# Performance work log

Measured on AMD Instinct MI355X. Metric: run time of the kernel, lower is better.

Reference implementation:

```python
import jax, jax.numpy as jnp
import numpy as np

BN_EPS = 1e-5

def _conv(x, w, b, pad):
    # x [B,C,H,W], w [O,I,kh,kw]
    y = jax.lax.conv_general_dilated(x, w, window_strides=(1, 1),
                                     padding=[(pad, pad), (pad, pad)],
                                     dimension_numbers=('NCHW', 'OIHW', 'NCHW'))
    return y + b[None, :, None, None]

def _bn(x, p):
    # p [4,C] rows: gamma, beta, running_mean, running_var (inference-mode BN)
    g, b, m, v = p
    scale = (g * jax.lax.rsqrt(v + BN_EPS))[None, :, None, None]
    return (x - m[None, :, None, None]) * scale + b[None, :, None, None]

def _up2_bilinear_ac(x):
    # UpsamplingBilinear2d(scale_factor=2) == bilinear, align_corners=True
    def interp(x, axis):
        n = x.shape[axis]
        out = 2 * n
        c = jnp.arange(out, dtype=x.dtype) * ((n - 1) / (out - 1))
        i0 = jnp.floor(c).astype(jnp.int32)
        i1 = jnp.minimum(i0 + 1, n - 1)
        w = c - i0.astype(x.dtype)
        sh = [1] * x.ndim
        sh[axis] = out
        w = w.reshape(sh)
        return jnp.take(x, i0, axis=axis) * (1 - w) + jnp.take(x, i1, axis=axis) * w
    return interp(interp(x, 2), 3)

def _dilate(x, k, iterations):
    # cv2.dilate with ones(k,k) kernel == sliding-window max (the custom-kernel target);
    # get_open_map detaches, hence stop_gradient.
    for _ in range(iterations):
        x = jax.lax.reduce_window(x, -jnp.inf, jax.lax.max,
                                  (1, 1, k, k), (1, 1, 1, 1), 'SAME')
    return jax.lax.stop_gradient(x)

def _pixel_shuffle2(x):
    B, C4, H, W = x.shape
    C = C4 // 4
    x = x.reshape(B, C, 2, 2, H, W).transpose(0, 1, 4, 2, 5, 3)
    return x.reshape(B, C, 2 * H, 2 * W)

def setup_inputs() -> dict:
    key = jax.random.key(0)
    ks = jax.random.split(key, 16)
    B, C1, C2, H, W = 8, 64, 128, 64, 64

    def bn_params(k, C):
        k1, k2, k3, k4 = jax.random.split(k, 4)
        g = jax.random.uniform(k1, (C,)) * 0.5 + 0.75
        b = jax.random.normal(k2, (C,)) * 0.1
        m = jax.random.normal(k3, (C,)) * 0.1
        v = jax.random.uniform(k4, (C,)) + 0.5
        return jnp.stack([g, b, m, v])

    def conv_w(k, o, i, kk):
        return jax.random.normal(k, (o, i, kk, kk)) * 0.05

    return {
        'cur_x': jax.random.normal(ks[0], (B, C1, 2 * H, 2 * W)),
        'dep_x': jax.random.normal(ks[1], (B, C2, H, W)),
        'in_map': jax.random.normal(ks[2], (B, 1, H, W)),
        'up_w': conv_w(ks[3], 4 * C1, C2, 7), 'up_b': jnp.zeros((4 * C1,)),
        'up_bn': bn_params(ks[4], 4 * C1),
        'conv2_w': conv_w(ks[5], C1, C1, 3), 'conv2_b': jnp.zeros((C1,)),
        'd1_w': conv_w(ks[6], C1, C1, 3), 'd1_b': jnp.zeros((C1,)),
        'd1_bn': bn_params(ks[7], C1),
        'd2_w': conv_w(ks[8], C1, C1, 3), 'd2_b': jnp.zeros((C1,)),
        'd2_bn': bn_params(ks[9], C1),
        'd3_w': conv_w(ks[10], C1, C1, 3), 'd3_b': jnp.zeros((C1,)),
        'd3_bn': bn_params(ks[11], C1),
        'out_w': conv_w(ks[12], 1, C1, 7), 'out_b': jnp.zeros((1,)),
        'beta': jnp.ones((1,)),
    }

def reference(cur_x, dep_x, in_map, up_w, up_b, up_bn, conv2_w, conv2_b,
              d1_w, d1_b, d1_bn, d2_w, d2_b, d2_bn, d3_w, d3_b, d3_bn,
              out_w, out_b, beta):
    K, IT = 3, 1  # opr_kernel_size, iterations
    # up + pixel shuffle: [B,C2,H,W] -> [B,C1,2H,2W]
    dep = _pixel_shuffle2(jax.nn.relu(_bn(_conv(dep_x, up_w, up_b, 3), up_bn)))
    in_map1 = 1.0 - in_map
    input_map = jax.nn.sigmoid(_up2_bilinear_ac(in_map))
    input_map1 = jax.nn.sigmoid(_up2_bilinear_ac(in_map1))
    increase_map = _dilate(input_map, K, IT) - input_map
    increase_map1 = _dilate(increase_map, K, IT) - increase_map
    increase_map2 = _dilate(input_map1, K, IT) - input_map1
    outmap = increase_map + increase_map1 + increase_map2
    fn = _conv(outmap * cur_x, conv2_w, conv2_b, 1)
    r = jax.nn.relu(_bn(_conv(dep + beta * fn, d1_w, d1_b, 1), d1_bn))
    r = jax.nn.relu(_bn(_conv(r, d2_w, d2_b, 1), d2_bn))
    r = jax.nn.relu(_bn(_conv(r, d3_w, d3_b, 1), d3_bn))
    output_map = _conv(r, out_w, out_b, 3)
    return (r, output_map)
```

## Files before the change

### kernel.cpp

```cpp
#include <hip/hip_runtime.h>
#include <hip/hip_bf16.h>
#include <math.h>

static __device__ __forceinline__ float sigm(float x) { return 1.0f / (1.0f + expf(-x)); }

static __device__ __forceinline__ short f2bf_s(float f) {
    unsigned u = __float_as_uint(f);
    u += 0x7fffu + ((u >> 16) & 1u);
    return (short)(u >> 16);
}
static __device__ __forceinline__ float bfb2f(short s) {
    return __uint_as_float(((unsigned)(unsigned short)s) << 16);
}

typedef __attribute__((ext_vector_type(8))) short short8;
typedef __attribute__((ext_vector_type(4))) short short4v;
typedef __attribute__((ext_vector_type(4))) float f32x4;

static __device__ __forceinline__ void gl_lds16(const void* g, void* l) {
    __builtin_amdgcn_global_load_lds(
        (const __attribute__((address_space(1))) unsigned int*)g,
        (__attribute__((address_space(3))) unsigned int*)l, 16, 0, 0);
}

__global__ __launch_bounds__(256) void k_maps(const float* __restrict__ in_map,
                                              short* __restrict__ om_bf) {
    __shared__ float s_u[20][20];
    __shared__ float s_inc[18][18];
    int tid = threadIdx.x;
    int b = blockIdx.z;
    int ty0 = (blockIdx.x >> 3) << 4, tx0 = (blockIdx.x & 7) << 4;
    const float* p = in_map + (b << 12);
    const float s = 63.0f / 127.0f;
    for (int e = tid; e < 400; e += 256) {
        int yy = e / 20, xx = e % 20;
        int gy = ty0 + yy - 2, gx = tx0 + xx - 2;
        float v = 0.0f;
        if ((unsigned)gy < 128u && (unsigned)gx < 128u) {
            float cy = gy * s, cx = gx * s;
            int iy0 = (int)cy, ix0 = (int)cx;
            float wy = cy - (float)iy0, wx = cx - (float)ix0;
            int iy1 = min(iy0 + 1, 63), ix1 = min(ix0 + 1, 63);
            float v00 = p[(iy0 << 6) + ix0], v01 = p[(iy0 << 6) + ix1];
            float v10 = p[(iy1 << 6) + ix0], v11 = p[(iy1 << 6) + ix1];
            v = (1.0f - wy) * ((1.0f - wx) * v00 + wx * v01) +
                wy          * ((1.0f - wx) * v10 + wx * v11);
        }
        s_u[yy][xx] = v;
    }
    __syncthreads();
    for (int e = tid; e < 324; e += 256) {
        int yy = e / 18, xx = e % 18;
        int gy = ty0 + yy - 1, gx = tx0 + xx - 1;
        float val = -INFINITY;
        if ((unsigned)gy < 128u && (unsigned)gx < 128u) {
            float uc = s_u[yy + 1][xx + 1];
            float mx = -INFINITY;
            for (int dy = -1; dy <= 1; ++dy) {
                int ny = gy + dy; if ((unsigned)ny >= 128u) continue;
                for (int dx = -1; dx <= 1; ++dx) {
                    int nx = gx + dx; if ((unsigned)nx >= 128u) continue;
                    mx = fmaxf(mx, s_u[yy + 1 + dy][xx + 1 + dx]);
                }
            }
            val = sigm(mx) - sigm(uc);
        }
        s_inc[yy][xx] = val;
    }
    __syncthreads();
    int row = tid >> 4, col = tid & 15;
    int gy = ty0 + row, gx = tx0 + col;
    float mx = -INFINITY;
    #pragma unroll
    for (int dy = 0; dy < 3; ++dy)
        #pragma unroll
        for (int dx = 0; dx < 3; ++dx)
            mx = fmaxf(mx, s_inc[row + dy][col + dx]);
    float uc = s_u[row + 2][col + 2];
    float mn = INFINITY;
    for (int dy = -1; dy <= 1; ++dy) {
        int ny = gy + dy; if ((unsigned)ny >= 128u) continue;
        for (int dx = -1; dx <= 1; ++dx) {
            int nx = gx + dx; if ((unsigned)nx >= 128u) continue;
            mn = fminf(mn, s_u[row + 2 + dy][col + 2 + dx]);
        }
    }
    float inc2 = sigm(1.0f - mn) - sigm(1.0f - uc);
    om_bf[(b << 14) + (gy << 7) + gx] = f2bf_s(mx + inc2);
}

__global__ __launch_bounds__(256) void k_premult(const float* __restrict__ cur_x,
                                                 const short* __restrict__ om_bf,
                                                 short* __restrict__ xin2) {
    int e = blockIdx.x * 256 + threadIdx.x;
    int flat = e << 2;
    int pix = flat & 16383;
    int b = flat >> 20;
    f32x4 xv = *(const f32x4*)&cur_x[flat];
    short4v ov = *(const short4v*)&om_bf[(b << 14) + pix];
    short4v res;
    #pragma unroll
    for (int k = 0; k < 4; ++k) res[k] = f2bf_s(xv[k] * bfb2f(ov[k]));
    *(short4v*)&xin2[flat] = res;
}

__global__ __launch_bounds__(256) void k_prepw3(const float* __restrict__ w0,
                                                const float* __restrict__ w1,
                                                const float* __restrict__ w2,
                                                const float* __restrict__ w3,
                                                short* __restrict__ wb3) {
    int s = blockIdx.x * 256 + threadIdx.x;
    if (s >= 147456) return;
    int layer = s / 36864; int r = s - layer * 36864;
    const float* w = (layer == 0) ? w0 : (layer == 1) ? w1 : (layer == 2) ? w2 : w3;
    int o = r / 576; int rem = r - o * 576;
    int c = rem / 9; int t = rem - c * 9;
    int dy = t / 3, dx = t - dy * 3;
    int cc = c >> 5, cl = c & 31;
    wb3[layer * 36864 + (((cc * 3 + dx) * 3 + dy) * 64 + o) * 32 + cl] = f2bf_s(w[r]);
}

__global__ __launch_bounds__(256) void k_prepw(const float* __restrict__ w,
                                               short* __restrict__ wb) {
    int s = blockIdx.x * 256 + threadIdx.x;
    if (s >= 1605632) return;
    int O = s / 6272; int r = s - O * 6272;
    int C = r / 49;   int T = r - C * 49;
    int dy = T / 7, dx = T - dy * 7;
    int nt = O >> 6, o = O & 63;
    int cc = C >> 5, c = C & 31;
    int W = ((((nt * 4 + cc) * 7 + dx) * 7 + dy) * 64 + o) * 32 + c;
    wb[W] = f2bf_s(w[s]);
}

__global__ __launch_bounds__(256) void k_prepx(const float* __restrict__ x,
                                               short* __restrict__ px) {
    int b = blockIdx.z;
    int yp = blockIdx.x;
    int tid = threadIdx.x;
    int y = yp - 3;
    bool inY = (unsigned)y < 64u;
    for (int cc = 0; cc < 4; ++cc) {
        short* orow = px + (((long)(b * 4 + cc) * 70 + yp) * 70) * 40;
        for (int e = tid; e < 350; e += 256) {
            int p = e / 70, xp = e - p * 70;
            int xg = xp - 3;
            short8 v = (short8){0, 0, 0, 0, 0, 0, 0, 0};
            if (p < 4 && inY && (unsigned)xg < 64u) {
                const float* src = x + (((b * 128 + cc * 32 + p * 8) << 12)) + (y << 6) + xg;
                #pragma unroll
                for (int i = 0; i < 8; ++i) v[i] = f2bf_s(src[i << 12]);
            }
            *(short8*)&orow[xp * 40 + p * 8] = v;
        }
    }
}

__global__ __launch_bounds__(512, 4) void k_upconv_mfma(
    const short* __restrict__ px,
    const short* __restrict__ wb,
    const float* __restrict__ cb,
    const float* __restrict__ bnp,
    short* __restrict__ dep) {
    __shared__ __attribute__((aligned(16))) short s_in[19360];
    int tid = threadIdx.x;
    int wave = tid >> 6, lane = tid & 63;
    int q = lane >> 4, m = lane & 15;
    int mw = wave & 3, ng = wave >> 2;
    int ty0 = (blockIdx.x >> 2) * 16;
    int tx0 = (blockIdx.x & 3) * 16;
    int nt = blockIdx.y;
    int b = blockIdx.z;
    f32x4 acc[4][2];
    #pragma unroll
    for (int i = 0; i < 4; ++i)
        #pragma unroll
        for (int j = 0; j < 2; ++j)
            acc[i][j] = (f32x4){0.f, 0.f, 0.f, 0.f};

    auto stage = [&](int cc) {
        const short* pxcc = px + ((((long)(b * 4 + cc) * 70 + ty0) * 70 + tx0) * 40);
        for (int c0 = (wave << 6); c0 < 2420; c0 += 512) {
            int chunk = c0 + lane;
            int row = chunk / 110;
            int k = chunk - row * 110;
            if (chunk < 2420)
                gl_lds16(pxcc + row * 2800 + (k << 3), &s_in[c0 << 3]);
        }
    };

    for (int cc = 0; cc < 4; ++cc) {
        if (cc) __syncthreads();
        stage(cc);
        __syncthreads();
        const short* sb = &s_in[0];
        const short* wcc = wb + ((nt * 4 + cc) * 49) * 2048;
        #pragma unroll 1
        for (int dx = 0; dx < 7; ++dx) {
            short8 a10[10];
            #pragma unroll
            for (int r = 0; r < 10; ++r)
                a10[r] = *(const short8*)&sb[((mw * 4 + r) * 22 + m + dx) * 40 + q * 8];
            const short* wdx = wcc + ((dx * 7) << 11);
            short8 wf[7];
            #pragma unroll
            for (int dy = 0; dy < 7; ++dy)
                wf[dy] = *(const short8*)(wdx + (dy << 11) + ((ng * 32 + m) << 5) + (q << 3));
            #pragma unroll
            for (int dy = 0; dy < 7; ++dy)
                #pragma unroll
                for (int i = 0; i < 4; ++i)
                    acc[i][0] = __builtin_amdgcn_mfma_f32_16x16x32_bf16(
                        a10[i + dy], wf[dy], acc[i][0], 0, 0, 0);
            #pragma unroll
            for (int dy = 0; dy < 7; ++dy)
                wf[dy] = *(const short8*)(wdx + (dy << 11) + ((ng * 32 + 16 + m) << 5) + (q << 3));
            #pragma unroll
            for (int dy = 0; dy < 7; ++dy)
                #pragma unroll
                for (int i = 0; i < 4; ++i)
                    acc[i][1] = __builtin_amdgcn_mfma_f32_16x16x32_bf16(
                        a10[i + dy], wf[dy], acc[i][1], 0, 0, 0);
        }
    }
    #pragma unroll
    for (int j = 0; j < 2; ++j) {
        int o = nt * 64 + ng * 32 + j * 16 + m;
        float g  = bnp[o],       bt = bnp[256 + o];
        float mn = bnp[512 + o], vv = bnp[768 + o];
        float scale = g * rsqrtf(vv + 1e-5f);
        float cbf = cb[o];
        int c = o >> 2, sbit = (o >> 1) & 1, tbit = o & 1;
        #pragma unroll
        for (int i = 0; i < 4; ++i) {
            int y = ty0 + mw * 4 + i;
            #pragma unroll
            for (int reg = 0; reg < 4; ++reg) {
                int xc = tx0 + q * 4 + reg;
                float val = (acc[i][j][reg] + cbf - mn) * scale + bt;
                val = fmaxf(val, 0.0f);
                dep[((b * 64 + c) << 14) + ((2 * y + sbit) << 7) + (2 * xc + tbit)] = f2bf_s(val);
            }
        }
    }
}

template <int MODE, bool OUTBF>
__global__ __launch_bounds__(256, 4) void k_conv3m(
    const short* __restrict__ xin,
    const short* __restrict__ wl,
    const short* __restrict__ dep,
    const float* __restrict__ cb,
    const float* __restrict__ bnp,
    const float* __restrict__ beta,
    void* __restrict__ out) {
    __shared__ __attribute__((aligned(16))) short s_in[180 * 40];
    int tid = threadIdx.x;
    int wave = tid >> 6, lane = tid & 63;
    int q = lane >> 4, m = lane & 15;
    int mw = wave >> 1, nw = wave & 1;
    int ty0 = (blockIdx.x >> 3) * 8;
    int tx0 = (blockIdx.x & 7) * 16;
    int b = blockIdx.z;
    f32x4 acc[4][2];
    #pragma unroll
    for (int i = 0; i < 4; ++i)
        #pragma unroll
        for (int j = 0; j < 2; ++j)
            acc[i][j] = (f32x4){0.f, 0.f, 0.f, 0.f};
    const short* xb = xin + ((long)(b * 64) << 14);
    for (int cc = 0; cc < 2; ++cc) {
        __syncthreads();
        for (int e = tid; e < 240; e += 256) {
            int cq = e / 60; int rem = e - cq * 60;
            int yy = rem / 6; int g = rem - yy * 6;
            int gy = ty0 + yy - 1;
            int gx0 = tx0 - 4 + (g << 2);
            short4v v[8];
            if ((unsigned)gy < 128u && (unsigned)gx0 < 128u) {
                const short* src = xb + ((cc * 32 + cq * 8) << 14) + (gy << 7) + gx0;
                #pragma unroll
                for (int j2 = 0; j2 < 8; ++j2) v[j2] = *(const short4v*)(src + (j2 << 14));
            } else {
                #pragma unroll
                for (int j2 = 0; j2 < 8; ++j2) v[j2] = (short4v){0, 0, 0, 0};
            }
            #pragma unroll
            for (int t = 0; t < 4; ++t) {
                int xx = (g << 2) - 3 + t;
                if ((unsigned)xx < 18u) {
                    short8 pk;
                    #pragma unroll
                    for (int j2 = 0; j2 < 8; ++j2) pk[j2] = v[j2][t];
                    *(short8*)&s_in[(yy * 18 + xx) * 40 + cq * 8] = pk;
                }
            }
        }
        __syncthreads();
        #pragma unroll 1
        for (int dx = 0; dx < 3; ++dx) {
            short8 a6[6];
            #pragma unroll
            for (int r = 0; r < 6; ++r)
                a6[r] = *(const short8*)&s_in[((mw * 4 + r) * 18 + m + dx) * 40 + q * 8];
            const short* wdx = wl + (((cc * 3 + dx) * 3) << 11);
            short8 wf[3];
            #pragma unroll
            for (int dy = 0; dy < 3; ++dy)
                wf[dy] = *(const short8*)(wdx + (dy << 11) + ((nw * 32 + m) << 5) + (q << 3));
            #pragma unroll
            for (int dy = 0; dy < 3; ++dy)
                #pragma unroll
                for (int i = 0; i < 4; ++i)
                    acc[i][0] = __builtin_amdgcn_mfma_f32_16x16x32_bf16(
                        a6[i + dy], wf[dy], acc[i][0], 0, 0, 0);
            #pragma unroll
            for (int dy = 0; dy < 3; ++dy)
                wf[dy] = *(const short8*)(wdx + (dy << 11) + ((nw * 32 + 16 + m) << 5) + (q << 3));
            #pragma unroll
            for (int dy = 0; dy < 3; ++dy)
                #pragma unroll
                for (int i = 0; i < 4; ++i)
                    acc[i][1] = __builtin_amdgcn_mfma_f32_16x16x32_bf16(
                        a6[i + dy], wf[dy], acc[i][1], 0, 0, 0);
        }
    }
    float betav = (MODE == 1) ? beta[0] : 0.0f;
    #pragma unroll
    for (int j = 0; j < 2; ++j) {
        int o = nw * 32 + j * 16 + m;
        float cbf = cb[o];
        float scale = 1.0f, shift = 0.0f;
        if (MODE == 0) {
            float g  = bnp[o],       bt = bnp[64 + o];
            float mm = bnp[128 + o], vv = bnp[192 + o];
            scale = g * rsqrtf(vv + 1e-5f);
            shift = bt - mm * scale;
        }
        #pragma unroll
        for (int i = 0; i < 4; ++i) {
            int y = ty0 + mw * 4 + i;
            int base = ((b * 64 + o) << 14) + (y << 7) + tx0 + q * 4;
            float vals[4];
            if (MODE == 1) {
                short4v dv = *(const short4v*)&dep[base];
                #pragma unroll
                for (int reg = 0; reg < 4; ++reg)
                    vals[reg] = bfb2f(dv[reg]) + betav * (acc[i][j][reg] + cbf);
            } else {
                #pragma unroll
                for (int reg = 0; reg < 4; ++reg)
                    vals[reg] = fmaxf((acc[i][j][reg] + cbf) * scale + shift, 0.0f);
            }
            if (OUTBF) {
                short4v sv;
                #pragma unroll
                for (int reg = 0; reg < 4; ++reg) sv[reg] = f2bf_s(vals[reg]);
                *(short4v*)((short*)out + base) = sv;
            } else {
                f32x4 fv;
                #pragma unroll
                for (int reg = 0; reg < 4; ++reg) fv[reg] = vals[reg];
                *(f32x4*)((float*)out + base) = fv;
            }
        }
    }
}

__global__ __launch_bounds__(256) void k_outconv(
    const float* __restrict__ r,
    const float* __restrict__ w,
    const float* __restrict__ ob,
    float* __restrict__ out) {
    __shared__ float s_in[8][22][22];
    int tid = threadIdx.x;
    int ty = tid >> 4, tx = tid & 15;
    int ty0 = (blockIdx.x >> 3) << 4, tx0 = (blockIdx.x & 7) << 4;
    int b = blockIdx.z;
    float acc4[4] = {0.f, 0.f, 0.f, 0.f};
    for (int c0 = 0; c0 < 64; c0 += 8) {
        __syncthreads();
        for (int e = tid; e < 8 * 484; e += 256) {
            int i = e / 484; int r2 = e - i * 484; int yy = r2 / 22; int xx = r2 - yy * 22;
            int gy = ty0 + yy - 3, gx = tx0 + xx - 3;
            float v = 0.0f;
            if ((unsigned)gy < 128u && (unsigned)gx < 128u)
                v = r[((b * 64 + c0 + i) << 14) + (gy << 7) + gx];
            s_in[i][yy][xx] = v;
        }
        __syncthreads();
        for (int i = 0; i < 8; ++i) {
            const float* wrow = w + (c0 + i) * 49;
            #pragma unroll
            for (int dy = 0; dy < 7; ++dy)
                #pragma unroll
                for (int dx = 0; dx < 7; ++dx)
                    acc4[i & 3] = fmaf(s_in[i][ty + dy][tx + dx], wrow[dy * 7 + dx], acc4[i & 3]);
        }
    }
    out[(b << 14) + ((ty0 + ty) << 7) + tx0 + tx] =
        (acc4[0] + acc4[1]) + (acc4[2] + acc4[3]) + ob[0];
}

extern "C" void kernel_launch(void* const* d_in, const int* in_sizes, int n_in,
                              void* d_out, int out_size, void* d_ws, size_t ws_size,
                              hipStream_t stream) {
    const float* cur_x  = (const float*)d_in[0];
    const float* dep_x  = (const float*)d_in[1];
    const float* in_map = (const float*)d_in[2];
    const float* up_w   = (const float*)d_in[3];
    const float* up_b   = (const float*)d_in[4];
    const float* up_bn  = (const float*)d_in[5];
    const float* c2_w   = (const float*)d_in[6];
    const float* c2_b   = (const float*)d_in[7];
    const float* d1_w   = (const float*)d_in[8];
    const float* d1_b   = (const float*)d_in[9];
    const float* d1_bn  = (const float*)d_in[10];
    const float* d2_w   = (const float*)d_in[11];
    const float* d2_b   = (const float*)d_in[12];
    const float* d2_bn  = (const float*)d_in[13];
    const float* d3_w   = (const float*)d_in[14];
    const float* d3_b   = (const float*)d_in[15];
    const float* d3_bn  = (const float*)d_in[16];
    const float* out_w  = (const float*)d_in[17];
    const float* out_b  = (const float*)d_in[18];
    const float* beta   = (const float*)d_in[19];

    char* ob = (char*)d_out;
    float* r_out  = (float*)ob;
    short* A      = (short*)d_ws;
    short* B      = (short*)ob;
    short* C      = (short*)(ob + 16777216);
    short* wb     = C;
    short* px     = wb + 1605632;
    short* om_bf  = (short*)(ob + 33554432);
    short* wb3    = (short*)(ob + 33554432);
    float* mapout = (float*)(ob + 33554432);

    k_maps<<<dim3(64, 1, 8), 256, 0, stream>>>(in_map, om_bf);
    k_premult<<<8192, 256, 0, stream>>>(cur_x, om_bf, A);
    k_prepw3<<<576, 256, 0, stream>>>(c2_w, d1_w, d2_w, d3_w, wb3);
    k_prepw<<<6272, 256, 0, stream>>>(up_w, wb);
    k_prepx<<<dim3(70, 1, 8), 256, 0, stream>>>(dep_x, px);
    k_upconv_mfma<<<dim3(16, 4, 8), 512, 0, stream>>>(px, wb, up_b, up_bn, B);
    k_conv3m<1, true><<<dim3(128, 1, 8), 256, 0, stream>>>(
        A, wb3 + 0 * 36864, B, c2_b, nullptr, beta, C);
    k_conv3m<0, true><<<dim3(128, 1, 8), 256, 0, stream>>>(
        C, wb3 + 1 * 36864, nullptr, d1_b, d1_bn, nullptr, B);
    k_conv3m<0, true><<<dim3(128, 1, 8), 256, 0, stream>>>(
        B, wb3 + 2 * 36864, nullptr, d2_b, d2_bn, nullptr, A);
    k_conv3m<0, false><<<dim3(128, 1, 8), 256, 0, stream>>>(
        A, wb3 + 3 * 36864, nullptr, d3_b, d3_bn, nullptr, r_out);
    k_outconv<<<dim3(64, 1, 8), 256, 0, stream>>>(r_out, out_w, out_b, mapout);
}
```

Baseline: 465.0 us.

## Merge prep kernels into one launch and retile 3x3 convs to 16-row tiles

Folds the map, weight-reorder, and input-padding prep kernels into a single kernel that dispatches work by block index, removing three launches. The 3x3 conv kernel now uses 512 threads covering a 16x16 tile, loads all 64 input channels into LDS once with a single barrier, and splits output channels across wave groups. This cuts launch overhead and the per-channel-chunk sync and reload in the conv, at the cost of a much larger LDS footprint per block (about 57KB), which may lower occupancy. The om_bf buffer is moved to a new offset in the scratch space.

```diff
diff --git a/kernel.cpp b/kernel.cpp
--- a/kernel.cpp
+++ b/kernel.cpp
@@ -23,70 +23,117 @@
         (__attribute__((address_space(3))) unsigned int*)l, 16, 0, 0);
 }
 
-__global__ __launch_bounds__(256) void k_maps(const float* __restrict__ in_map,
-                                              short* __restrict__ om_bf) {
+__global__ __launch_bounds__(256) void k_prep_all(
+    const float* __restrict__ in_map, short* __restrict__ om_bf,
+    const float* __restrict__ w0, const float* __restrict__ w1,
+    const float* __restrict__ w2, const float* __restrict__ w3,
+    short* __restrict__ wb3,
+    const float* __restrict__ up_w, short* __restrict__ wb,
+    const float* __restrict__ dep_x, short* __restrict__ px) {
     __shared__ float s_u[20][20];
     __shared__ float s_inc[18][18];
+    int blk = blockIdx.x;
     int tid = threadIdx.x;
-    int b = blockIdx.z;
-    int ty0 = (blockIdx.x >> 3) << 4, tx0 = (blockIdx.x & 7) << 4;
-    const float* p = in_map + (b << 12);
-    const float s = 63.0f / 127.0f;
-    for (int e = tid; e < 400; e += 256) {
-        int yy = e / 20, xx = e % 20;
-        int gy = ty0 + yy - 2, gx = tx0 + xx - 2;
-        float v = 0.0f;
-        if ((unsigned)gy < 128u && (unsigned)gx < 128u) {
-            float cy = gy * s, cx = gx * s;
-            int iy0 = (int)cy, ix0 = (int)cx;
-            float wy = cy - (float)iy0, wx = cx - (float)ix0;
-            int iy1 = min(iy0 + 1, 63), ix1 = min(ix0 + 1, 63);
-            float v00 = p[(iy0 << 6) + ix0], v01 = p[(iy0 << 6) + ix1];
-            float v10 = p[(iy1 << 6) + ix0], v11 = p[(iy1 << 6) + ix1];
-            v = (1.0f - wy) * ((1.0f - wx) * v00 + wx * v01) +
-                wy          * ((1.0f - wx) * v10 + wx * v11);
-        }
-        s_u[yy][xx] = v;
-    }
-    __syncthreads();
-    for (int e = tid; e < 324; e += 256) {
-        int yy = e / 18, xx = e % 18;
-        int gy = ty0 + yy - 1, gx = tx0 + xx - 1;
-        float val = -INFINITY;
-        if ((unsigned)gy < 128u && (unsigned)gx < 128u) {
-            float uc = s_u[yy + 1][xx + 1];
-            float mx = -INFINITY;
-            for (int dy = -1; dy <= 1; ++dy) {
-                int ny = gy + dy; if ((unsigned)ny >= 128u) continue;
-                for (int dx = -1; dx <= 1; ++dx) {
-                    int nx = gx + dx; if ((unsigned)nx >= 128u) continue;
-                    mx = fmaxf(mx, s_u[yy + 1 + dy][xx + 1 + dx]);
+
+    if (blk < 512) {
+        int b = blk >> 6;
+        int inner = blk & 63;
+        int ty0 = (inner >> 3) << 4, tx0 = (inner & 7) << 4;
+        const float* p = in_map + (b << 12);
+        const float s = 63.0f / 127.0f;
+        for (int e = tid; e < 400; e += 256) {
+            int yy = e / 20, xx = e % 20;
+            int gy = ty0 + yy - 2, gx = tx0 + xx - 2;
+            float v = 0.0f;
+            if ((unsigned)gy < 128u && (unsigned)gx < 128u) {
+                float cy = gy * s, cx = gx * s;
+                int iy0 = (int)cy, ix0 = (int)cx;
+                float wy = cy - (float)iy0, wx = cx - (float)ix0;
+                int iy1 = min(iy0 + 1, 63), ix1 = min(ix0 + 1, 63);
+                float v00 = p[(iy0 << 6) + ix0], v01 = p[(iy0 << 6) + ix1];
+                float v10 = p[(iy1 << 6) + ix0], v11 = p[(iy1 << 6) + ix1];
+                v = (1.0f - wy) * ((1.0f - wx) * v00 + wx * v01) +
+                    wy          * ((1.0f - wx) * v10 + wx * v11);
+            }
+            s_u[yy][xx] = v;
+        }
+        __syncthreads();
+        for (int e = tid; e < 324; e += 256) {
+            int yy = e / 18, xx = e % 18;
+            int gy = ty0 + yy - 1, gx = tx0 + xx - 1;
+            float val = -INFINITY;
+            if ((unsigned)gy < 128u && (unsigned)gx < 128u) {
+                float uc = s_u[yy + 1][xx + 1];
+                float mx = -INFINITY;
+                for (int dy = -1; dy <= 1; ++dy) {
+                    int ny = gy + dy; if ((unsigned)ny >= 128u) continue;
+                    for (int dx = -1; dx <= 1; ++dx) {
+                        int nx = gx + dx; if ((unsigned)nx >= 128u) continue;
+                        mx = fmaxf(mx, s_u[yy + 1 + dy][xx + 1 + dx]);
+                    }
                 }
-            }
-            val = sigm(mx) - sigm(uc);
-        }
-        s_inc[yy][xx] = val;
-    }
-    __syncthreads();
-    int row = tid >> 4, col = tid & 15;
-    int gy = ty0 + row, gx = tx0 + col;
-    float mx = -INFINITY;
-    #pragma unroll
-    for (int dy = 0; dy < 3; ++dy)
-        #pragma unroll
-        for (int dx = 0; dx < 3; ++dx)
-            mx = fmaxf(mx, s_inc[row + dy][col + dx]);
-    float uc = s_u[row + 2][col + 2];
-    float mn = INFINITY;
-    for (int dy = -1; dy <= 1; ++dy) {
-        int ny = gy + dy; if ((unsigned)ny >= 128u) continue;
-        for (int dx = -1; dx <= 1; ++dx) {
-            int nx = gx + dx; if ((unsigned)nx >= 128u) continue;
-            mn = fminf(mn, s_u[row + 2 + dy][col + 2 + dx]);
-        }
-    }
-    float inc2 = sigm(1.0f - mn) - sigm(1.0f - uc);
-    om_bf[(b << 14) + (gy << 7) + gx] = f2bf_s(mx + inc2);
+                val = sigm(mx) - sigm(uc);
+            }
+            s_inc[yy][xx] = val;
+        }
+        __syncthreads();
+        int row = tid >> 4, col = tid & 15;
+        int gy = ty0 + row, gx = tx0 + col;
+        float mx = -INFINITY;
+        #pragma unroll
+        for (int dy = 0; dy < 3; ++dy)
+            #pragma unroll
+            for (int dx = 0; dx < 3; ++dx)
+                mx = fmaxf(mx, s_inc[row + dy][col + dx]);
+        float uc = s_u[row + 2][col + 2];
+        float mn = INFINITY;
+        for (int dy = -1; dy <= 1; ++dy) {
+            int ny = gy + dy; if ((unsigned)ny >= 128u) continue;
+            for (int dx = -1; dx <= 1; ++dx) {
+                int nx = gx + dx; if ((unsigned)nx >= 128u) continue;
+                mn = fminf(mn, s_u[row + 2 + dy][col + 2 + dx]);
+            }
+        }
+        float inc2 = sigm(1.0f - mn) - sigm(1.0f - uc);
+        om_bf[(b << 14) + (gy << 7) + gx] = f2bf_s(mx + inc2);
+    } else if (blk < 1088) {
+        int s = (blk - 512) * 256 + tid;
+        int layer = s / 36864; int r = s - layer * 36864;
+        const float* w = (layer == 0) ? w0 : (layer == 1) ? w1 : (layer == 2) ? w2 : w3;
+        int o = r / 576; int rem = r - o * 576;
+        int c = rem / 9; int t = rem - c * 9;
+        int dy = t / 3, dx = t - dy * 3;
+        int cc = c >> 5, cl = c & 31;
+        wb3[layer * 36864 + (((cc * 3 + dx) * 3 + dy) * 64 + o) * 32 + cl] = f2bf_s(w[r]);
+    } else if (blk < 7360) {
+        int s = (blk - 1088) * 256 + tid;
+        int O = s / 6272; int r = s - O * 6272;
+        int C = r / 49;   int T = r - C * 49;
+        int dy = T / 7, dx = T - dy * 7;
+        int nt = O >> 6, o = O & 63;
+        int cc = C >> 5, c = C & 31;
+        int W = ((((nt * 4 + cc) * 7 + dx) * 7 + dy) * 64 + o) * 32 + c;
+        wb[W] = f2bf_s(up_w[s]);
+    } else {
+        int idx = blk - 7360;
+        int b = idx / 70, yp = idx - (idx / 70) * 70;
+        int y = yp - 3;
+        bool inY = (unsigned)y < 64u;
+        for (int cc = 0; cc < 4; ++cc) {
+            short* orow = px + (((long)(b * 4 + cc) * 70 + yp) * 70) * 40;
+            for (int e = tid; e < 350; e += 256) {
+                int p2 = e / 70, xp = e - p2 * 70;
+                int xg = xp - 3;
+                short8 v = (short8){0, 0, 0, 0, 0, 0, 0, 0};
+                if (p2 < 4 && inY && (unsigned)xg < 64u) {
+                    const float* src = dep_x + (((b * 128 + cc * 32 + p2 * 8) << 12)) + (y << 6) + xg;
+                    #pragma unroll
+                    for (int i = 0; i < 8; ++i) v[i] = f2bf_s(src[i << 12]);
+                }
+                *(short8*)&orow[xp * 40 + p2 * 8] = v;
+            }
+        }
+    }
 }
 
 __global__ __launch_bounds__(256) void k_premult(const float* __restrict__ cur_x,
@@ -102,58 +149,6 @@
     #pragma unroll
     for (int k = 0; k < 4; ++k) res[k] = f2bf_s(xv[k] * bfb2f(ov[k]));
     *(short4v*)&xin2[flat] = res;
-}
-
-__global__ __launch_bounds__(256) void k_prepw3(const float* __restrict__ w0,
-                                                const float* __restrict__ w1,
-                                                const float* __restrict__ w2,
-                                                const float* __restrict__ w3,
-                                                short* __restrict__ wb3) {
-    int s = blockIdx.x * 256 + threadIdx.x;
-    if (s >= 147456) return;
-    int layer = s / 36864; int r = s - layer * 36864;
-    const float* w = (layer == 0) ? w0 : (layer == 1) ? w1 : (layer == 2) ? w2 : w3;
-    int o = r / 576; int rem = r - o * 576;
-    int c = rem / 9; int t = rem - c * 9;
-    int dy = t / 3, dx = t - dy * 3;
-    int cc = c >> 5, cl = c & 31;
-    wb3[layer * 36864 + (((cc * 3 + dx) * 3 + dy) * 64 + o) * 32 + cl] = f2bf_s(w[r]);
-}
-
-__global__ __launch_bounds__(256) void k_prepw(const float* __restrict__ w,
-                                               short* __restrict__ wb) {
-    int s = blockIdx.x * 256 + threadIdx.x;
-    if (s >= 1605632) return;
-    int O = s / 6272; int r = s - O * 6272;
-    int C = r / 49;   int T = r - C * 49;
-    int dy = T / 7, dx = T - dy * 7;
-    int nt = O >> 6, o = O & 63;
-    int cc = C >> 5, c = C & 31;
-    int W = ((((nt * 4 + cc) * 7 + dx) * 7 + dy) * 64 + o) * 32 + c;
-    wb[W] = f2bf_s(w[s]);
-}
-
-__global__ __launch_bounds__(256) void k_prepx(const float* __restrict__ x,
-                                               short* __restrict__ px) {
-    int b = blockIdx.z;
-    int yp = blockIdx.x;
-    int tid = threadIdx.x;
-    int y = yp - 3;
-    bool inY = (unsigned)y < 64u;
-    for (int cc = 0; cc < 4; ++cc) {
-        short* orow = px + (((long)(b * 4 + cc) * 70 + yp) * 70) * 40;
-        for (int e = tid; e < 350; e += 256) {
-            int p = e / 70, xp = e - p * 70;
-            int xg = xp - 3;
-            short8 v = (short8){0, 0, 0, 0, 0, 0, 0, 0};
-            if (p < 4 && inY && (unsigned)xg < 64u) {
-                const float* src = x + (((b * 128 + cc * 32 + p * 8) << 12)) + (y << 6) + xg;
-                #pragma unroll
-                for (int i = 0; i < 8; ++i) v[i] = f2bf_s(src[i << 12]);
-            }
-            *(short8*)&orow[xp * 40 + p * 8] = v;
-        }
-    }
 }
 
 __global__ __launch_bounds__(512, 4) void k_upconv_mfma(
@@ -246,7 +241,7 @@
 }
 
 template <int MODE, bool OUTBF>
-__global__ __launch_bounds__(256, 4) void k_conv3m(
+__global__ __launch_bounds__(512, 4) void k_conv3m(
     const short* __restrict__ xin,
     const short* __restrict__ wl,
     const short* __restrict__ dep,
@@ -254,12 +249,12 @@
     const float* __restrict__ bnp,
     const float* __restrict__ beta,
     void* __restrict__ out) {
-    __shared__ __attribute__((aligned(16))) short s_in[180 * 40];
+    __shared__ __attribute__((aligned(16))) short s_in[324 * 88];
     int tid = threadIdx.x;
     int wave = tid >> 6, lane = tid & 63;
     int q = lane >> 4, m = lane & 15;
-    int mw = wave >> 1, nw = wave & 1;
-    int ty0 = (blockIdx.x >> 3) * 8;
+    int mw = wave & 3, og = wave >> 2;
+    int ty0 = (blockIdx.x >> 3) * 16;
     int tx0 = (blockIdx.x & 7) * 16;
     int b = blockIdx.z;
     f32x4 acc[4][2];
@@ -269,45 +264,45 @@
         for (int j = 0; j < 2; ++j)
             acc[i][j] = (f32x4){0.f, 0.f, 0.f, 0.f};
     const short* xb = xin + ((long)(b * 64) << 14);
+    for (int e = tid; e < 864; e += 512) {
+        int cq = e / 108; int rem = e - cq * 108;
+        int yy = rem / 6; int g = rem - yy * 6;
+        int gy = ty0 + yy - 1;
+        int gx0 = tx0 - 4 + (g << 2);
+        short4v v[8];
+        if ((unsigned)gy < 128u && (unsigned)gx0 < 128u) {
+            const short* src = xb + ((cq * 8) << 14) + (gy << 7) + gx0;
+            #pragma unroll
+            for (int j2 = 0; j2 < 8; ++j2) v[j2] = *(const short4v*)(src + (j2 << 14));
+        } else {
+            #pragma unroll
+            for (int j2 = 0; j2 < 8; ++j2) v[j2] = (short4v){0, 0, 0, 0};
+        }
+        #pragma unroll
+        for (int t = 0; t < 4; ++t) {
+            int xx = (g << 2) - 3 + t;
+            if ((unsigned)xx < 18u) {
+                short8 pk;
+                #pragma unroll
+                for (int j2 = 0; j2 < 8; ++j2) pk[j2] = v[j2][t];
+                *(short8*)&s_in[(yy * 18 + xx) * 88 + cq * 8] = pk;
+            }
+        }
+    }
+    __syncthreads();
+    #pragma unroll 1
     for (int cc = 0; cc < 2; ++cc) {
-        __syncthreads();
-        for (int e = tid; e < 240; e += 256) {
-            int cq = e / 60; int rem = e - cq * 60;
-            int yy = rem / 6; int g = rem - yy * 6;
-            int gy = ty0 + yy - 1;
-            int gx0 = tx0 - 4 + (g << 2);
-            short4v v[8];
-            if ((unsigned)gy < 128u && (unsigned)gx0 < 128u) {
-                const short* src = xb + ((cc * 32 + cq * 8) << 14) + (gy << 7) + gx0;
-                #pragma unroll
-                for (int j2 = 0; j2 < 8; ++j2) v[j2] = *(const short4v*)(src + (j2 << 14));
-            } else {
-                #pragma unroll
-                for (int j2 = 0; j2 < 8; ++j2) v[j2] = (short4v){0, 0, 0, 0};
-            }
-            #pragma unroll
-            for (int t = 0; t < 4; ++t) {
-                int xx = (g << 2) - 3 + t;
-                if ((unsigned)xx < 18u) {
-                    short8 pk;
-                    #pragma unroll
-                    for (int j2 = 0; j2 < 8; ++j2) pk[j2] = v[j2][t];
-                    *(short8*)&s_in[(yy * 18 + xx) * 40 + cq * 8] = pk;
-                }
-            }
-        }
-        __syncthreads();
         #pragma unroll 1
         for (int dx = 0; dx < 3; ++dx) {
             short8 a6[6];
             #pragma unroll
             for (int r = 0; r < 6; ++r)
-                a6[r] = *(const short8*)&s_in[((mw * 4 + r) * 18 + m + dx) * 40 + q * 8];
+                a6[r] = *(const short8*)&s_in[((mw * 4 + r) * 18 + m + dx) * 88 + cc * 32 + q * 8];
             const short* wdx = wl + (((cc * 3 + dx) * 3) << 11);
             short8 wf[3];
             #pragma unroll
             for (int dy = 0; dy < 3; ++dy)
-                wf[dy] = *(const short8*)(wdx + (dy << 11) + ((nw * 32 + m) << 5) + (q << 3));
+                wf[dy] = *(const short8*)(wdx + (dy << 11) + ((og * 32 + m) << 5) + (q << 3));
             #pragma unroll
             for (int dy = 0; dy < 3; ++dy)
                 #pragma unroll
@@ -316,7 +311,7 @@
                         a6[i + dy], wf[dy], acc[i][0], 0, 0, 0);
             #pragma unroll
             for (int dy = 0; dy < 3; ++dy)
-                wf[dy] = *(const short8*)(wdx + (dy << 11) + ((nw * 32 + 16 + m) << 5) + (q << 3));
+                wf[dy] = *(const short8*)(wdx + (dy << 11) + ((og * 32 + 16 + m) << 5) + (q << 3));
             #pragma unroll
             for (int dy = 0; dy < 3; ++dy)
                 #pragma unroll
@@ -328,7 +323,7 @@
     float betav = (MODE == 1) ? beta[0] : 0.0f;
     #pragma unroll
     for (int j = 0; j < 2; ++j) {
-        int o = nw * 32 + j * 16 + m;
+        int o = og * 32 + j * 16 + m;
         float cbf = cb[o];
         float scale = 1.0f, shift = 0.0f;
         if (MODE == 0) {
@@ -433,23 +428,21 @@
     short* C      = (short*)(ob + 16777216);
     short* wb     = C;
     short* px     = wb + 1605632;
-    short* om_bf  = (short*)(ob + 33554432);
+    short* om_bf  = (short*)(ob + 32532480);
     short* wb3    = (short*)(ob + 33554432);
     float* mapout = (float*)(ob + 33554432);
 
-    k_maps<<<dim3(64, 1, 8), 256, 0, stream>>>(in_map, om_bf);
+    k_prep_all<<<7920, 256, 0, stream>>>(in_map, om_bf, c2_w, d1_w, d2_w, d3_w, wb3,
+                                         up_w, wb, dep_x, px);
     k_premult<<<8192, 256, 0, stream>>>(cur_x, om_bf, A);
-    k_prepw3<<<576, 256, 0, stream>>>(c2_w, d1_w, d2_w, d3_w, wb3);
-    k_prepw<<<6272, 256, 0, stream>>>(up_w, wb);
-    k_prepx<<<dim3(70, 1, 8), 256, 0, stream>>>(dep_x, px);
     k_upconv_mfma<<<dim3(16, 4, 8), 512, 0, stream>>>(px, wb, up_b, up_bn, B);
-    k_conv3m<1, true><<<dim3(128, 1, 8), 256, 0, stream>>>(
+    k_conv3m<1, true><<<dim3(64, 1, 8), 512, 0, stream>>>(
         A, wb3 + 0 * 36864, B, c2_b, nullptr, beta, C);
-    k_conv3m<0, true><<<dim3(128, 1, 8), 256, 0, stream>>>(
+    k_conv3m<0, true><<<dim3(64, 1, 8), 512, 0, stream>>>(
         C, wb3 + 1 * 36864, nullptr, d1_b, d1_bn, nullptr, B);
-    k_conv3m<0, true><<<dim3(128, 1, 8), 256, 0, stream>>>(
+    k_conv3m<0, true><<<dim3(64, 1, 8), 512, 0, stream>>>(
         B, wb3 + 2 * 36864, nullptr, d2_b, d2_bn, nullptr, A);
-    k_conv3m<0, false><<<dim3(128, 1, 8), 256, 0, stream>>>(
+    k_conv3m<0, false><<<dim3(64, 1, 8), 512, 0, stream>>>(
         A, wb3 + 3 * 36864, nullptr, d3_b, d3_bn, nullptr, r_out);
     k_outconv<<<dim3(64, 1, 8), 256, 0, stream>>>(r_out, out_w, out_b, mapout);
 }
```

Result: no change. 463.8 us (-0.3%).
